# Kernel tuning notes

Measured on AMD Instinct MI355X. Metric: run time of the kernel, lower is better.

The kernel has to match this reference:

```python
import jax, jax.numpy as jnp
import numpy as np
import math

NUM_HEADS = 16
HEAD_DIM = 64
D_MODEL = NUM_HEADS * HEAD_DIM  # 1024
B, S = 4, 2048

def setup_inputs() -> dict:
    key = jax.random.key(0)
    ks = jax.random.split(key, 8)
    sd = 1.0 / math.sqrt(D_MODEL)
    return {
        "hidden_states": jax.random.normal(ks[0], (B, S, D_MODEL), jnp.float32),
        "attention_mask": jnp.zeros((B, 1, 1, S), jnp.float32),
        "Wq": jax.random.normal(ks[1], (D_MODEL, D_MODEL), jnp.float32) * sd,
        "bq": jnp.zeros((D_MODEL,), jnp.float32),
        "Wk": jax.random.normal(ks[2], (D_MODEL, D_MODEL), jnp.float32) * sd,
        "bk": jnp.zeros((D_MODEL,), jnp.float32),
        "Wv": jax.random.normal(ks[3], (D_MODEL, D_MODEL), jnp.float32) * sd,
        "bv": jnp.zeros((D_MODEL,), jnp.float32),
    }

def _split_heads(x):
    # [B, S, D] -> [B, H, S, hd]
    b, s, _ = x.shape
    return x.reshape(b, s, NUM_HEADS, HEAD_DIM).transpose(0, 2, 1, 3)

def reference(hidden_states, attention_mask, Wq, bq, Wk, bk, Wv, bv):
    # Linear projections (torch nn.Linear: x @ W.T + b)
    q = _split_heads(hidden_states @ Wq.T + bq)
    k = _split_heads(hidden_states @ Wk.T + bk)
    v = _split_heads(hidden_states @ Wv.T + bv)
    scale = 1.0 / math.sqrt(HEAD_DIM)
    # [B, H, Sq, Sk] attention scores, fully materialized as in the original
    scores = jnp.einsum("bhqd,bhkd->bhqk", q, k) * scale + attention_mask
    # relusq replacement for softmax
    probs = jnp.square(jax.nn.relu(scores))
    ctx = jnp.einsum("bhqk,bhkd->bhqd", probs, v)  # [B, H, S, hd]
    b = ctx.shape[0]
    return ctx.transpose(0, 2, 1, 3).reshape(b, -1, D_MODEL)
```

## Files before the change

kernel.cpp:

```cpp
#include <hip/hip_runtime.h>


typedef __bf16 bf16x8 __attribute__((ext_vector_type(8)));
typedef __bf16 bf16x4 __attribute__((ext_vector_type(4)));
typedef short  s16x4  __attribute__((ext_vector_type(4)));
typedef float  f32x4  __attribute__((ext_vector_type(4)));
typedef float  floatx4 __attribute__((ext_vector_type(4)));

#define MFMA16(a, b, c) __builtin_amdgcn_mfma_f32_16x16x32_bf16(a, b, c, 0, 0, 0)
#define MFMA16K16(a, b, c) \
    __builtin_amdgcn_mfma_f32_16x16x16bf16_1k(a, b, c, 0, 0, 0)

#define WAITCNT_VM2() __builtin_amdgcn_s_waitcnt(0x0F72)
#define WAITCNT_VM4() __builtin_amdgcn_s_waitcnt(0x0F74)
#define BARRIER() __builtin_amdgcn_s_barrier()
#define SETPRIO(p) __builtin_amdgcn_s_setprio(p)

__device__ __forceinline__ void glds16(const __bf16* g, __bf16* l) {
    __builtin_amdgcn_global_load_lds(
        (const __attribute__((address_space(1))) void*)g,
        (__attribute__((address_space(3))) void*)l, 16, 0, 0);
}

__global__ __launch_bounds__(256) void convert_kernel(
    const float* __restrict__ X, const float* __restrict__ Wq,
    const float* __restrict__ Wk, const float* __restrict__ Wv,
    __bf16* __restrict__ Xb, __bf16* __restrict__ Wqb,
    __bf16* __restrict__ Wkb, __bf16* __restrict__ Wvb)
{
    int blk = blockIdx.x;
    const float* src; __bf16* dst; size_t base;
    if (blk < 4096)      { src = X;  dst = Xb;  base = (size_t)blk * 2048; }
    else if (blk < 4608) { src = Wq; dst = Wqb; base = (size_t)(blk - 4096) * 2048; }
    else if (blk < 5120) { src = Wk; dst = Wkb; base = (size_t)(blk - 4608) * 2048; }
    else                 { src = Wv; dst = Wvb; base = (size_t)(blk - 5120) * 2048; }
    size_t off = base + (size_t)threadIdx.x * 8;
    floatx4 a = *(const floatx4*)(src + off);
    floatx4 c = *(const floatx4*)(src + off + 4);
    bf16x8 o;
    o[0] = (__bf16)a[0]; o[1] = (__bf16)a[1]; o[2] = (__bf16)a[2]; o[3] = (__bf16)a[3];
    o[4] = (__bf16)c[0]; o[5] = (__bf16)c[1]; o[6] = (__bf16)c[2]; o[7] = (__bf16)c[3];
    *(bf16x8*)(dst + off) = o;
}

__global__ __launch_bounds__(256) void qkv_gemm_kernel(
    const __bf16* __restrict__ Xb,
    const __bf16* __restrict__ Wqb, const __bf16* __restrict__ Wkb,
    const __bf16* __restrict__ Wvb,
    const float* __restrict__ bq, const float* __restrict__ bk,
    const float* __restrict__ bv,
    __bf16* __restrict__ qws, __bf16* __restrict__ kws, __bf16* __restrict__ vws)
{
    __shared__ __bf16 As[3][128 * 32];
    __shared__ __bf16 Bs[3][128 * 32];

    const int tid  = threadIdx.x;
    const int lane = tid & 63;
    const int wave = tid >> 6;
    const int wm   = (wave >> 1) * 64;
    const int wn   = (wave & 1) * 64;
    const int quad = lane >> 4;
    const int l16  = lane & 15;
    const int m0   = blockIdx.y * 128;

    const int sel = blockIdx.x >> 3;
    const bool vmode = (sel == 2);
    const __bf16* Wb = (sel == 0) ? Wqb : (sel == 1) ? Wkb : Wvb;
    const float* bias = (sel == 0) ? bq : (sel == 1) ? bk : bv;
    __bf16* outp = (sel == 0) ? qws : (sel == 1) ? kws : vws;
    const int n0 = (blockIdx.x & 7) * 128;

    const int woffA = vmode ? wm : wn;
    const int woffB = vmode ? wn : wm;

    const int srow = lane >> 2;
    const int schk = lane & 3;
    const int rchk = quad ^ ((l16 >> 1) & 3);

    f32x4 acc[4][4] = {};

    #pragma unroll
    for (int i = 0; i < 2; ++i) {
        int rb = wave * 32 + i * 16;
        int r  = rb + srow;
        int c  = schk ^ ((r >> 1) & 3);
        glds16(Xb + (size_t)(m0 + r) * 1024 + c * 8, &As[0][rb * 32]);
        glds16(Wb + (size_t)(n0 + r) * 1024 + c * 8, &Bs[0][rb * 32]);
    }

    int bc = 0, bn = 1, bx = 2;
    for (int s = 0; s < 32; ++s) {
        const int kn = ((s + 1) & 31) * 32;
        #pragma unroll
        for (int i = 0; i < 2; ++i) {
            int rb = wave * 32 + i * 16;
            int r  = rb + srow;
            int c  = schk ^ ((r >> 1) & 3);
            glds16(Xb + (size_t)(m0 + r) * 1024 + kn + c * 8, &As[bn][rb * 32]);
            glds16(Wb + (size_t)(n0 + r) * 1024 + kn + c * 8, &Bs[bn][rb * 32]);
        }
        WAITCNT_VM4();
        BARRIER();

        const __bf16* Pa_ = vmode ? &As[bc][0] : &Bs[bc][0];
        const __bf16* Pb_ = vmode ? &Bs[bc][0] : &As[bc][0];

        SETPRIO(1);
        bf16x8 af[4], bfr[4];
        #pragma unroll
        for (int a = 0; a < 4; ++a)
            af[a] = *(const bf16x8*)&Pa_[(woffA + a * 16 + l16) * 32 + rchk * 8];
        #pragma unroll
        for (int bb = 0; bb < 4; ++bb)
            bfr[bb] = *(const bf16x8*)&Pb_[(woffB + bb * 16 + l16) * 32 + rchk * 8];
        #pragma unroll
        for (int a = 0; a < 4; ++a)
            #pragma unroll
            for (int bb = 0; bb < 4; ++bb)
                acc[a][bb] = MFMA16(af[a], bfr[bb], acc[a][bb]);
        SETPRIO(0);

        int tmp = bc; bc = bn; bn = bx; bx = tmp;
    }

    if (!vmode) {
        #pragma unroll
        for (int a = 0; a < 4; ++a) {
            int n = n0 + woffA + a * 16 + quad * 4;
            floatx4 bv4 = *(const floatx4*)&bias[n];
            int h = n >> 6, d0 = n & 63;
            #pragma unroll
            for (int bb = 0; bb < 4; ++bb) {
                int m = m0 + woffB + bb * 16 + l16;
                int bt = m >> 11, ss = m & 2047;
                bf16x4 o;
                #pragma unroll
                for (int r = 0; r < 4; ++r)
                    o[r] = (__bf16)(acc[a][bb][r] + bv4[r]);
                *(bf16x4*)&outp[((size_t)(bt * 16 + h) * 2048 + ss) * 64 + d0] = o;
            }
        }
    } else {
        #pragma unroll
        for (int a = 0; a < 4; ++a) {
            int m = m0 + woffA + a * 16 + quad * 4;
            int bt = m >> 11, s0 = m & 2047;
            #pragma unroll
            for (int bb = 0; bb < 4; ++bb) {
                int n = n0 + woffB + bb * 16 + l16;
                float bvv = bias[n];
                int h = n >> 6, d = n & 63;
                bf16x4 o;
                #pragma unroll
                for (int r = 0; r < 4; ++r)
                    o[r] = (__bf16)(acc[a][bb][r] + bvv);
                *(bf16x4*)&outp[((size_t)(bt * 16 + h) * 64 + d) * 2048 + s0] = o;
            }
        }
    }
}

__global__ __launch_bounds__(512, 4) void attn_kernel(
    const __bf16* __restrict__ Q, const __bf16* __restrict__ K,
    const __bf16* __restrict__ Vt, const float* __restrict__ mask,
    float* __restrict__ out)
{
    __shared__ __bf16 Ks[2][64 * 64];
    __shared__ __bf16 Vs[2][64 * 64];
    __shared__ float  Ms[2048];

    const int tid  = threadIdx.x;
    const int lane = tid & 63;
    const int wave = tid >> 6;
    const int quad = lane >> 4;
    const int l16  = lane & 15;
    const int bh   = blockIdx.y;
    const int b    = bh >> 4;
    const int h    = bh & 15;
    const int q0   = blockIdx.x * 256 + wave * 32;

    const __bf16* Qb = Q  + (size_t)bh * 2048 * 64;
    const __bf16* Kb = K  + (size_t)bh * 2048 * 64;
    const __bf16* Vb = Vt + (size_t)bh * 64 * 2048;
    const float*  mb = mask + b * 2048;

    const int rb = wave * 8;
    const int sr = rb + (lane >> 3);
    const int sc = ((lane & 7) ^ (sr & 7)) * 8;

    bf16x8 aq[2][2];
    #pragma unroll
    for (int qi = 0; qi < 2; ++qi)
        #pragma unroll
        for (int kcd = 0; kcd < 2; ++kcd)
            aq[qi][kcd] = *(const bf16x8*)(Qb +
                (size_t)(q0 + qi * 16 + l16) * 64 + kcd * 32 + quad * 8);

    f32x4 co[2][4] = {};

    glds16(Kb + (size_t)sr * 64 + sc, &Ks[0][rb * 64]);
    glds16(Vb + (size_t)sr * 2048 + sc, &Vs[0][rb * 64]);
    glds16((const __bf16*)mb + (size_t)wave * 512 + lane * 8,
           (__bf16*)Ms + wave * 512);

    for (int t = 0; t < 32; ++t) {
        const int k0 = t * 64;
        const int kn = ((t + 1) & 31) * 64;
        const int nb = (t + 1) & 1;
        glds16(Kb + (size_t)(kn + sr) * 64 + sc, &Ks[nb][rb * 64]);
        glds16(Vb + (size_t)sr * 2048 + kn + sc, &Vs[nb][rb * 64]);
        WAITCNT_VM2();
        BARRIER();

        const __bf16* Kt = &Ks[t & 1][0];
        const __bf16* Vtile = &Vs[t & 1][0];

        f32x4 st[4][2] = {};
        SETPRIO(1);
        #pragma unroll
        for (int ki = 0; ki < 4; ++ki) {
            #pragma unroll
            for (int kcd = 0; kcd < 2; ++kcd) {
                int key = ki * 16 + l16;
                bf16x8 ak = *(const bf16x8*)&Kt[key * 64 +
                    (((kcd * 4 + quad) ^ (key & 7)) * 8)];
                #pragma unroll
                for (int qi = 0; qi < 2; ++qi)
                    st[ki][qi] = MFMA16(ak, aq[qi][kcd], st[ki][qi]);
            }
        }
        SETPRIO(0);

        bf16x4 pf[4][2];
        #pragma unroll
        for (int ki = 0; ki < 4; ++ki) {
            floatx4 mk = *(const floatx4*)&Ms[k0 + ki * 16 + quad * 4];
            #pragma unroll
            for (int qi = 0; qi < 2; ++qi) {
                bf16x4 pv;
                #pragma unroll
                for (int r = 0; r < 4; ++r) {
                    float x = st[ki][qi][r] * 0.125f + mk[r];
                    x = fmaxf(x, 0.0f);
                    pv[r] = (__bf16)(x * x);
                }
                pf[ki][qi] = pv;
            }
        }

        SETPRIO(1);
        #pragma unroll
        for (int ki = 0; ki < 4; ++ki) {
            bf16x4 vb4[4];
            #pragma unroll
            for (int dt = 0; dt < 4; ++dt) {
                int d = dt * 16 + l16;
                int g = ki * 2 + (quad >> 1);
                vb4[dt] = *(const bf16x4*)&Vtile[d * 64 +
                    ((g ^ (d & 7)) * 8) + (quad & 1) * 4];
            }
            #pragma unroll
            for (int qi = 0; qi < 2; ++qi) {
                s16x4 pa = __builtin_bit_cast(s16x4, pf[ki][qi]);
                #pragma unroll
                for (int dt = 0; dt < 4; ++dt)
                    co[qi][dt] = MFMA16K16(pa,
                        __builtin_bit_cast(s16x4, vb4[dt]), co[qi][dt]);
            }
        }
        SETPRIO(0);
        BARRIER();
    }

    #pragma unroll
    for (int qi = 0; qi < 2; ++qi)
        #pragma unroll
        for (int r = 0; r < 4; ++r) {
            int q = q0 + qi * 16 + quad * 4 + r;
            float* orow = &out[(((size_t)b * 2048 + q) * 16 + h) * 64];
            #pragma unroll
            for (int dt = 0; dt < 4; ++dt)
                orow[dt * 16 + l16] = co[qi][dt][r];
        }
}

extern "C" void kernel_launch(void* const* d_in, const int* in_sizes, int n_in,
                              void* d_out, int out_size, void* d_ws, size_t ws_size,
                              hipStream_t stream) {
    const float* hidden = (const float*)d_in[0];
    const float* mask   = (const float*)d_in[1];
    const float* Wq     = (const float*)d_in[2];
    const float* bq     = (const float*)d_in[3];
    const float* Wk     = (const float*)d_in[4];
    const float* bk     = (const float*)d_in[5];
    const float* Wv     = (const float*)d_in[6];
    const float* bv     = (const float*)d_in[7];
    float* out = (float*)d_out;

    __bf16* qws = (__bf16*)d_ws;
    __bf16* kws = qws + (size_t)64 * 2048 * 64;
    __bf16* vws = kws + (size_t)64 * 2048 * 64;
    __bf16* Xb  = vws + (size_t)64 * 2048 * 64;
    __bf16* Wqb = Xb  + (size_t)8192 * 1024;
    __bf16* Wkb = Wqb + (size_t)1024 * 1024;
    __bf16* Wvb = Wkb + (size_t)1024 * 1024;

    convert_kernel<<<dim3(5632), dim3(256), 0, stream>>>(hidden, Wq, Wk, Wv,
                                                         Xb, Wqb, Wkb, Wvb);
    qkv_gemm_kernel<<<dim3(24, 64), dim3(256), 0, stream>>>(Xb, Wqb, Wkb, Wvb,
                                                            bq, bk, bv,
                                                            qws, kws, vws);
    attn_kernel<<<dim3(8, 64), dim3(512), 0, stream>>>(qws, kws, vws, mask, out);
}
```

Measured before the change: 268.9 us.

## Widen QKV GEMM K-tile to 64 with double buffering and reorder attention grid

The QKV projection GEMM moves from a triple-buffered 32-wide K tile to a double-buffered 64-wide K tile, with an XOR swizzle over 8 chunks. Each tile is now loaded and then waited on fully at the end of the iteration, which halves the number of barriers per K loop but overlaps less of the load with compute. The attention kernel's grid is transposed so that consecutive blocks cover different heads rather than query tiles of the same head, which changes L2 locality for K/V. The relu-square epilogue is also written as vector operations.

```diff
diff --git a/kernel.cpp b/kernel.cpp
--- a/kernel.cpp
+++ b/kernel.cpp
@@ -11,8 +11,8 @@
 #define MFMA16K16(a, b, c) \
     __builtin_amdgcn_mfma_f32_16x16x16bf16_1k(a, b, c, 0, 0, 0)
 
+#define WAITCNT_VM0() __builtin_amdgcn_s_waitcnt(0x0F70)
 #define WAITCNT_VM2() __builtin_amdgcn_s_waitcnt(0x0F72)
-#define WAITCNT_VM4() __builtin_amdgcn_s_waitcnt(0x0F74)
 #define BARRIER() __builtin_amdgcn_s_barrier()
 #define SETPRIO(p) __builtin_amdgcn_s_setprio(p)
 
@@ -51,8 +51,8 @@
     const float* __restrict__ bv,
     __bf16* __restrict__ qws, __bf16* __restrict__ kws, __bf16* __restrict__ vws)
 {
-    __shared__ __bf16 As[3][128 * 32];
-    __shared__ __bf16 Bs[3][128 * 32];
+    __shared__ __bf16 As[2][128 * 64];
+    __shared__ __bf16 Bs[2][128 * 64];
 
     const int tid  = threadIdx.x;
     const int lane = tid & 63;
@@ -73,54 +73,60 @@
     const int woffA = vmode ? wm : wn;
     const int woffB = vmode ? wn : wm;
 
-    const int srow = lane >> 2;
-    const int schk = lane & 3;
-    const int rchk = quad ^ ((l16 >> 1) & 3);
+    const int srow = lane >> 3;
+    const int schk = lane & 7;
 
     f32x4 acc[4][4] = {};
 
     #pragma unroll
-    for (int i = 0; i < 2; ++i) {
-        int rb = wave * 32 + i * 16;
+    for (int i = 0; i < 4; ++i) {
+        int rb = wave * 32 + i * 8;
         int r  = rb + srow;
-        int c  = schk ^ ((r >> 1) & 3);
-        glds16(Xb + (size_t)(m0 + r) * 1024 + c * 8, &As[0][rb * 32]);
-        glds16(Wb + (size_t)(n0 + r) * 1024 + c * 8, &Bs[0][rb * 32]);
+        int c  = schk ^ (r & 7);
+        glds16(Xb + (size_t)(m0 + r) * 1024 + c * 8, &As[0][rb * 64]);
+        glds16(Wb + (size_t)(n0 + r) * 1024 + c * 8, &Bs[0][rb * 64]);
     }
-
-    int bc = 0, bn = 1, bx = 2;
-    for (int s = 0; s < 32; ++s) {
-        const int kn = ((s + 1) & 31) * 32;
-        #pragma unroll
-        for (int i = 0; i < 2; ++i) {
-            int rb = wave * 32 + i * 16;
+    WAITCNT_VM0();
+    BARRIER();
+
+    for (int s = 0; s < 16; ++s) {
+        const int kn = ((s + 1) & 15) * 64;
+        const int nb = (s + 1) & 1;
+        const int bc = s & 1;
+        #pragma unroll
+        for (int i = 0; i < 4; ++i) {
+            int rb = wave * 32 + i * 8;
             int r  = rb + srow;
-            int c  = schk ^ ((r >> 1) & 3);
-            glds16(Xb + (size_t)(m0 + r) * 1024 + kn + c * 8, &As[bn][rb * 32]);
-            glds16(Wb + (size_t)(n0 + r) * 1024 + kn + c * 8, &Bs[bn][rb * 32]);
-        }
-        WAITCNT_VM4();
-        BARRIER();
+            int c  = schk ^ (r & 7);
+            glds16(Xb + (size_t)(m0 + r) * 1024 + kn + c * 8, &As[nb][rb * 64]);
+            glds16(Wb + (size_t)(n0 + r) * 1024 + kn + c * 8, &Bs[nb][rb * 64]);
+        }
 
         const __bf16* Pa_ = vmode ? &As[bc][0] : &Bs[bc][0];
         const __bf16* Pb_ = vmode ? &Bs[bc][0] : &As[bc][0];
 
         SETPRIO(1);
-        bf16x8 af[4], bfr[4];
-        #pragma unroll
-        for (int a = 0; a < 4; ++a)
-            af[a] = *(const bf16x8*)&Pa_[(woffA + a * 16 + l16) * 32 + rchk * 8];
-        #pragma unroll
-        for (int bb = 0; bb < 4; ++bb)
-            bfr[bb] = *(const bf16x8*)&Pb_[(woffB + bb * 16 + l16) * 32 + rchk * 8];
-        #pragma unroll
-        for (int a = 0; a < 4; ++a)
+        #pragma unroll
+        for (int kk8 = 0; kk8 < 8; kk8 += 4) {
+            bf16x8 af[4], bfr[4];
+            #pragma unroll
+            for (int a = 0; a < 4; ++a)
+                af[a] = *(const bf16x8*)&Pa_[(woffA + a * 16 + l16) * 64 +
+                                             (((kk8 + quad) ^ (l16 & 7)) * 8)];
             #pragma unroll
             for (int bb = 0; bb < 4; ++bb)
-                acc[a][bb] = MFMA16(af[a], bfr[bb], acc[a][bb]);
+                bfr[bb] = *(const bf16x8*)&Pb_[(woffB + bb * 16 + l16) * 64 +
+                                               (((kk8 + quad) ^ (l16 & 7)) * 8)];
+            #pragma unroll
+            for (int a = 0; a < 4; ++a)
+                #pragma unroll
+                for (int bb = 0; bb < 4; ++bb)
+                    acc[a][bb] = MFMA16(af[a], bfr[bb], acc[a][bb]);
+        }
         SETPRIO(0);
 
-        int tmp = bc; bc = bn; bn = bx; bx = tmp;
+        WAITCNT_VM0();
+        BARRIER();
     }
 
     if (!vmode) {
@@ -174,10 +180,10 @@
     const int wave = tid >> 6;
     const int quad = lane >> 4;
     const int l16  = lane & 15;
-    const int bh   = blockIdx.y;
+    const int bh   = blockIdx.x;
     const int b    = bh >> 4;
     const int h    = bh & 15;
-    const int q0   = blockIdx.x * 256 + wave * 32;
+    const int q0   = blockIdx.y * 256 + wave * 32;
 
     const __bf16* Qb = Q  + (size_t)bh * 2048 * 64;
     const __bf16* Kb = K  + (size_t)bh * 2048 * 64;
@@ -232,18 +238,18 @@
         SETPRIO(0);
 
         bf16x4 pf[4][2];
+        const f32x4 zero4 = {};
         #pragma unroll
         for (int ki = 0; ki < 4; ++ki) {
-            floatx4 mk = *(const floatx4*)&Ms[k0 + ki * 16 + quad * 4];
+            f32x4 mk = *(const f32x4*)&Ms[k0 + ki * 16 + quad * 4];
             #pragma unroll
             for (int qi = 0; qi < 2; ++qi) {
+                f32x4 x = st[ki][qi] * 0.125f + mk;
+                x = __builtin_elementwise_max(x, zero4);
+                x = x * x;
                 bf16x4 pv;
-                #pragma unroll
-                for (int r = 0; r < 4; ++r) {
-                    float x = st[ki][qi][r] * 0.125f + mk[r];
-                    x = fmaxf(x, 0.0f);
-                    pv[r] = (__bf16)(x * x);
-                }
+                pv[0] = (__bf16)x[0]; pv[1] = (__bf16)x[1];
+                pv[2] = (__bf16)x[2]; pv[3] = (__bf16)x[3];
                 pf[ki][qi] = pv;
             }
         }
@@ -310,5 +316,5 @@
     qkv_gemm_kernel<<<dim3(24, 64), dim3(256), 0, stream>>>(Xb, Wqb, Wkb, Wvb,
                                                             bq, bk, bv,
                                                             qws, kws, vws);
-    attn_kernel<<<dim3(8, 64), dim3(512), 0, stream>>>(qws, kws, vws, mask, out);
-}
+    attn_kernel<<<dim3(64, 8), dim3(512), 0, stream>>>(qws, kws, vws, mask, out);
+}
```

Result: faster. 250.2 us (-6.9%).
